# Kernel tuning notes

Measured on AMD Instinct MI355X. Metric: run time of the kernel, lower is better.

The kernel has to match this reference:

```python
import jax, jax.numpy as jnp
import numpy as np
import math

VOCAB = 32000
HIDDEN = 256
N_HEADS = 8
HEAD_DIM = 32
MAX_LEN = 2048


def _pos_encoding(max_len, d_model, dtype=jnp.float32):
    # Matches PositionalEncoding buffer (even d_model).
    pos = jnp.arange(max_len, dtype=dtype)[:, None]                       # [L,1]
    div = jnp.exp(jnp.arange(0, d_model, 2, dtype=dtype) * (-(math.log(10000.0) / d_model)))
    ang = pos * div                                                        # [L, d/2]
    pe = jnp.zeros((max_len, d_model), dtype=dtype)
    pe = pe.at[:, 0::2].set(jnp.sin(ang))
    pe = pe.at[:, 1::2].set(jnp.cos(ang))
    return pe


def setup_inputs() -> dict:
    key = jax.random.key(0)
    ks = jax.random.split(key, 7)
    B, S = 8, 2047
    s = 0.02
    x = jax.random.randint(ks[0], (B, S), 0, VOCAB + 1, dtype=jnp.int64)
    emb_w = jax.random.normal(ks[1], (VOCAB + 1, HIDDEN), jnp.float32) * s
    wq = jax.random.normal(ks[2], (N_HEADS, HEAD_DIM, HIDDEN), jnp.float32) * s
    wk = jax.random.normal(ks[3], (N_HEADS, HEAD_DIM, HIDDEN), jnp.float32) * s
    wv = jax.random.normal(ks[4], (N_HEADS, HEAD_DIM, HIDDEN), jnp.float32) * s
    wo = jax.random.normal(ks[5], (HIDDEN, N_HEADS * HEAD_DIM), jnp.float32) * s
    wu = jax.random.normal(ks[6], (VOCAB + 1, HIDDEN), jnp.float32) * s
    return {"x": x, "emb_w": emb_w, "wq": wq, "wk": wk, "wv": wv, "wo": wo, "wu": wu}


def reference(x, emb_w, wq, wk, wv, wo, wu):
    B, S = x.shape
    # prepend CLS token (id=2)
    tok = jnp.concatenate([jnp.full((B, 1), 2, dtype=x.dtype), x], axis=1)  # [B, S+1]
    y = emb_w[tok]                                                          # [B, S+1, H]
    y = y + _pos_encoding(S + 1, HIDDEN, y.dtype)
    # batched per-head QKV (nn.Linear: out = in @ W.T)
    q = jnp.einsum('bsh,nkh->bnsk', y, wq)
    k = jnp.einsum('bsh,nkh->bnsk', y, wk)
    v = jnp.einsum('bsh,nkh->bnsk', y, wv)
    scores = jnp.einsum('bnsk,bntk->bnst', q, k) / (HEAD_DIM ** 0.5)        # [B,N,S+1,S+1]
    A = jax.nn.softmax(scores, axis=-1)
    o = jnp.einsum('bnst,bntk->bnsk', A, v)                                 # [B,N,S+1,K]
    o = jnp.transpose(o, (0, 2, 1, 3)).reshape(B, S + 1, N_HEADS * HEAD_DIM)
    att = o @ wo.T + y     # residual inside MultiHeadAttention
    y = att + y            # second residual in MultiHeadTransformerPosEmb.forward
    out = y[:, 0, :] @ wu.T                                                 # [B, VOCAB+1]
    return out
```

## Files before the change

kernel.cpp:

```cpp
#include <hip/hip_runtime.h>
#include <stdint.h>

#define B_   8
#define S_   2047
#define L_   2048
#define H_   256
#define NH_  8
#define HD_  32
#define V_   32001
#define NCH_ 128
#define TCH_ 16
#define GRID_ 1024
#define BAR_STRIDE_ 2048

__device__ __forceinline__ void ast(float* p, float v) {
    __hip_atomic_store((unsigned int*)p, __float_as_uint(v),
                       __ATOMIC_RELAXED, __HIP_MEMORY_SCOPE_AGENT);
}
__device__ __forceinline__ float ald(const float* p) {
    return __uint_as_float(__hip_atomic_load((const unsigned int*)p,
                           __ATOMIC_RELAXED, __HIP_MEMORY_SCOPE_AGENT));
}
__device__ __forceinline__ float foldx(float a, int off) {
    return a + __shfl_xor(a, off, 64);
}
__device__ __forceinline__ float sel8(const float a[8], int j) {
    float v = a[0];
    v = (j == 1) ? a[1] : v;
    v = (j == 2) ? a[2] : v;
    v = (j == 3) ? a[3] : v;
    v = (j == 4) ? a[4] : v;
    v = (j == 5) ? a[5] : v;
    v = (j == 6) ? a[6] : v;
    v = (j == 7) ? a[7] : v;
    return v;
}

__device__ __forceinline__ void gsync(unsigned int* bp, int bid) {
    __syncthreads();
    if (threadIdx.x == 0) {
        int sg = bid & 31;
        unsigned int* sub = bp + 16 + sg * 16;
        unsigned int* rel = bp + 528 + sg * 16;
        unsigned int prev = __hip_atomic_fetch_add(sub, 1u, __ATOMIC_RELAXED,
                                                   __HIP_MEMORY_SCOPE_AGENT);
        if (prev == 31u) {
            unsigned int m = __hip_atomic_fetch_add(bp, 1u, __ATOMIC_RELAXED,
                                                    __HIP_MEMORY_SCOPE_AGENT);
            if (m == 31u) {
                for (int i = 0; i < 32; ++i)
                    __hip_atomic_store(bp + 528 + i * 16, 1u, __ATOMIC_RELAXED,
                                       __HIP_MEMORY_SCOPE_AGENT);
            }
        }
        while (__hip_atomic_load(rel, __ATOMIC_RELAXED,
                                 __HIP_MEMORY_SCOPE_AGENT) == 0u)
            __builtin_amdgcn_s_sleep(2);
    }
    __syncthreads();
}

__global__ __launch_bounds__(256, 4) void mega(const int* __restrict__ x,
                                               const float* __restrict__ emb,
                                               const float* __restrict__ wq,
                                               const float* __restrict__ wk,
                                               const float* __restrict__ wv,
                                               const float* __restrict__ wo,
                                               const float* __restrict__ wu,
                                               float* __restrict__ out,
                                               float* __restrict__ qk,
                                               float* __restrict__ z,
                                               float* __restrict__ o_g,
                                               float* __restrict__ esum_blk,
                                               float* __restrict__ psum,
                                               unsigned int* __restrict__ bars) {
    int bid = blockIdx.x, tid = threadIdx.x;

    __shared__ float smem[4][2056];
    float* smf = &smem[0][0];

    if (bid < NH_) {
        int n = bid;
        float* y0l = smem[0];
        float* q0p = smem[1];
        float* q0l = smem[2];
        float v = emb[2 * H_ + tid] + ((tid & 1) ? 1.0f : 0.0f);
        y0l[tid] = v;
        __syncthreads();
        {
            int k = tid >> 3, part = tid & 7;
            const float* w = wq + (n * HD_ + k) * H_ + part * 32;
            const float* yy = y0l + part * 32;
            float acc = 0.f;
#pragma unroll
            for (int j = 0; j < 32; ++j) acc += w[j] * yy[j];
            q0p[k * 8 + part] = acc;
        }
        __syncthreads();
        if (tid < HD_) {
            float s = 0.f;
#pragma unroll
            for (int j = 0; j < 8; ++j) s += q0p[tid * 8 + j];
            q0l[tid] = s;
        }
        __syncthreads();
        float acc = 0.f;
        for (int k = 0; k < HD_; ++k)
            acc += q0l[k] * wk[(n * HD_ + k) * H_ + tid];
        ast(qk + n * H_ + tid, acc * 0.17677669529663687f);
    }
    gsync(bars + 0 * BAR_STRIDE_, bid);

    {
        int b = bid >> 7, c = bid & 127;
        int lane = tid & 63, w = tid >> 6;
        int h0 = lane * 4;

        for (int i = tid; i < NH_ * H_; i += 256)
            smem[3][i] = ald(qk + i);
        __syncthreads();

        float4 qr[NH_];
#pragma unroll
        for (int n = 0; n < NH_; ++n)
            qr[n] = *(const float4*)&smem[3][n * H_ + h0];
        __syncthreads();

        const float cdiv = 0.07195578414202881f;
        float div0 = __expf(-(float)(lane * 2) * cdiv);
        float div1 = __expf(-(float)(lane * 2 + 1) * cdiv);

        float4 acc[NH_];
        float es[NH_];
#pragma unroll
        for (int n = 0; n < NH_; ++n) {
            acc[n] = make_float4(0.f, 0.f, 0.f, 0.f);
            es[n] = 0.f;
        }

        int t0 = c * TCH_ + w * 4;
        int toks[4];
#pragma unroll
        for (int i = 0; i < 4; ++i) {
            int t = t0 + i;
            toks[i] = (t == 0) ? 2 : x[b * S_ + t - 1];
        }

#pragma unroll
        for (int i = 0; i < 4; ++i) {
            int t = t0 + i;
            float4 ev = *(const float4*)(emb + (size_t)toks[i] * H_ + h0);
            float a0 = (float)t * div0, a1 = (float)t * div1;
            float4 y4;
            y4.x = ev.x + __sinf(a0); y4.y = ev.y + __cosf(a0);
            y4.z = ev.z + __sinf(a1); y4.w = ev.w + __cosf(a1);

            float a[NH_];
#pragma unroll
            for (int n = 0; n < NH_; ++n)
                a[n] = qr[n].x * y4.x + qr[n].y * y4.y + qr[n].z * y4.z + qr[n].w * y4.w;

            float m4[4];
#pragma unroll
            for (int k = 0; k < 4; ++k) {
                float lo = foldx(a[k], 32), hi = foldx(a[k + 4], 32);
                m4[k] = (lane & 32) ? hi : lo;
            }
            float m2[2];
#pragma unroll
            for (int k = 0; k < 2; ++k) {
                float lo = foldx(m4[k], 16), hi = foldx(m4[k + 2], 16);
                m2[k] = (lane & 16) ? hi : lo;
            }
            float lo = foldx(m2[0], 8), hi = foldx(m2[1], 8);
            float m1 = (lane & 8) ? hi : lo;
            m1 = foldx(m1, 4); m1 = foldx(m1, 2); m1 = foldx(m1, 1);
            float e = __expf(m1);

#pragma unroll
            for (int n = 0; n < NH_; ++n) {
                float en = __shfl(e, n * 8, 64);
                acc[n].x += en * y4.x; acc[n].y += en * y4.y;
                acc[n].z += en * y4.z; acc[n].w += en * y4.w;
                es[n] += en;
            }
        }

#pragma unroll
        for (int n = 0; n < NH_; ++n)
            *(float4*)&smem[w][n * H_ + h0] = acc[n];
        if (lane < NH_) smem[w][2048 + lane] = sel8(es, lane);
        __syncthreads();

#pragma unroll
        for (int jj = 0; jj < (NH_ * H_) / 256; ++jj) {
            int j = jj * 256 + tid;
            ast(psum + (size_t)bid * (NH_ * H_) + j,
                smem[0][j] + smem[1][j] + smem[2][j] + smem[3][j]);
        }
        if (tid < NH_)
            ast(esum_blk + bid * NH_ + tid,
                smem[0][2048 + tid] + smem[1][2048 + tid]
              + smem[2][2048 + tid] + smem[3][2048 + tid]);
    }
    gsync(bars + 1 * BAR_STRIDE_, bid);

    if (bid < 64) {
        int b = bid >> 3, n = bid & 7;
        float* ybar  = smem[0];
        float* opb   = smem[1];
        float* es128 = smem[2];
        if (tid < 128)
            es128[tid] = ald(esum_blk + (size_t)(b * NCH_ + tid) * NH_ + n);
        __syncthreads();
        if (tid < 64) {
            float v = es128[tid] + es128[tid + 64];
#pragma unroll
            for (int off = 32; off > 0; off >>= 1) v += __shfl_xor(v, off, 64);
            if (tid == 0) es128[192] = 1.0f / v;
        }
        __syncthreads();
        {
            const float* pp = psum + (size_t)(b * NCH_) * (NH_ * H_) + n * H_ + tid;
            float s = 0.f;
#pragma unroll 16
            for (int cc = 0; cc < NCH_; ++cc) s += ald(pp + (size_t)cc * NH_ * H_);
            ybar[tid] = s * es128[192];
        }
        __syncthreads();
        {
            int k = tid >> 3, p = tid & 7;
            const float* wrow = wv + (size_t)(n * HD_ + k) * H_ + p * 32;
            const float* yy = ybar + p * 32;
            float s = 0.f;
#pragma unroll
            for (int j = 0; j < 32; ++j) s += wrow[j] * yy[j];
            opb[k * 8 + p] = s;
        }
        __syncthreads();
        if (tid < HD_) {
            float s = 0.f;
#pragma unroll
            for (int p = 0; p < 8; ++p) s += opb[tid * 8 + p];
            ast(o_g + b * (NH_ * HD_) + n * HD_ + tid, s);
        }
    }
    gsync(bars + 2 * BAR_STRIDE_, bid);

    if (bid < B_) {
        int b = bid;
        float* o_l = smem[0];
        o_l[tid] = ald(o_g + b * (NH_ * HD_) + tid);
        float y0v = emb[2 * H_ + tid] + ((tid & 1) ? 1.0f : 0.0f);
        __syncthreads();
        const float* wrow = wo + (size_t)tid * (NH_ * HD_);
        float s = 0.f;
#pragma unroll 16
        for (int j4 = 0; j4 < (NH_ * HD_) / 4; ++j4) {
            float4 w4 = *(const float4*)(wrow + j4 * 4);
            s += w4.x * o_l[j4 * 4] + w4.y * o_l[j4 * 4 + 1]
               + w4.z * o_l[j4 * 4 + 2] + w4.w * o_l[j4 * 4 + 3];
        }
        ast(z + b * H_ + tid, s + 2.0f * y0v);
    }
    gsync(bars + 3 * BAR_STRIDE_, bid);

    if (bid < (V_ + 63) / 64) {
        int lane = tid & 63, w = tid >> 6;
        int m = lane & 15;
        int g = lane >> 4;
        float* zs = smf;
        float* sm_out = smf + 2560;
        for (int i = tid; i < B_ * H_; i += 256) {
            int b = i >> 8, h = i & 255;
            zs[b * 320 + (h >> 4) * 20 + (h & 15)] = ald(z + i);
        }
        __syncthreads();

        int base = bid * 64;
#pragma unroll
        for (int pass = 0; pass < 4; ++pass) {
            int rl = w * 16 + pass * 4 + g;
            int v = base + rl;
            int vc = (v < V_) ? v : (V_ - 1);
            const float* wr = wu + (size_t)vc * H_ + m * 16;
            float4 w0 = *(const float4*)(wr);
            float4 w1 = *(const float4*)(wr + 4);
            float4 w2 = *(const float4*)(wr + 8);
            float4 w3 = *(const float4*)(wr + 12);
            float acc[B_];
#pragma unroll
            for (int b = 0; b < B_; ++b) {
                const float* zb = zs + b * 320 + m * 20;
                float4 z0 = *(const float4*)(zb);
                float4 z1 = *(const float4*)(zb + 4);
                float4 z2 = *(const float4*)(zb + 8);
                float4 z3 = *(const float4*)(zb + 12);
                acc[b] = z0.x * w0.x + z0.y * w0.y + z0.z * w0.z + z0.w * w0.w
                       + z1.x * w1.x + z1.y * w1.y + z1.z * w1.z + z1.w * w1.w
                       + z2.x * w2.x + z2.y * w2.y + z2.z * w2.z + z2.w * w2.w
                       + z3.x * w3.x + z3.y * w3.y + z3.z * w3.z + z3.w * w3.w;
            }
#pragma unroll
            for (int off = 1; off <= 8; off <<= 1) {
#pragma unroll
                for (int b = 0; b < B_; ++b) acc[b] += __shfl_xor(acc[b], off, 64);
            }
            if (m < B_) sm_out[m * 65 + rl] = sel8(acc, m);
        }
        __syncthreads();
        for (int i = tid; i < B_ * 64; i += 256) {
            int b = i >> 6, vl = i & 63, v = base + vl;
            if (v < V_) out[b * V_ + v] = sm_out[b * 65 + vl];
        }
    }
}

extern "C" void kernel_launch(void* const* d_in, const int* in_sizes, int n_in,
                              void* d_out, int out_size, void* d_ws, size_t ws_size,
                              hipStream_t stream) {
    const int*   x   = (const int*)d_in[0];
    const float* emb = (const float*)d_in[1];
    const float* wq  = (const float*)d_in[2];
    const float* wk  = (const float*)d_in[3];
    const float* wv  = (const float*)d_in[4];
    const float* wo  = (const float*)d_in[5];
    const float* wu  = (const float*)d_in[6];
    float*       out = (float*)d_out;

    float* qk       = (float*)d_ws;
    float* z        = qk + NH_ * H_;
    float* o_g      = z + B_ * H_;
    float* esum_blk = o_g + B_ * NH_ * HD_;
    float* psum     = esum_blk + GRID_ * NH_;
    unsigned int* bars = (unsigned int*)(psum + (size_t)GRID_ * NH_ * H_);

    hipMemsetAsync(bars, 0, 4 * BAR_STRIDE_ * sizeof(unsigned int), stream);

    mega<<<GRID_, 256, 0, stream>>>(x, emb, wq, wk, wv, wo, wu, out,
                                    qk, z, o_g, esum_blk, psum, bars);
}
```

Measured before the change: 146.9 us.

## Replace grid-wide barriers with targeted flag waits and double grid size

Removes the four full-grid barriers. Each stage now signals its consumers through counters or release flags, so blocks wait only on the data they need, and the unembedding weight rows are prefetched before the wait. The grid doubles to 2048 blocks with 8 tokens each and occupancy 8, and per-wave accumulators are replaced by LDS atomics. This raises occupancy and overlap, but spin-waiting depends on every block being co-resident, and the LDS atomics plus twice as many partial sums add contention and reduction work.

```diff
diff --git a/kernel.cpp b/kernel.cpp
--- a/kernel.cpp
+++ b/kernel.cpp
@@ -8,9 +8,9 @@
 #define NH_  8
 #define HD_  32
 #define V_   32001
-#define NCH_ 128
-#define TCH_ 16
-#define GRID_ 1024
+#define NCH_ 256
+#define TCH_ 8
+#define GRID_ 2048
 #define BAR_STRIDE_ 2048
 
 __device__ __forceinline__ void ast(float* p, float v) {
@@ -20,6 +20,12 @@
 __device__ __forceinline__ float ald(const float* p) {
     return __uint_as_float(__hip_atomic_load((const unsigned int*)p,
                            __ATOMIC_RELAXED, __HIP_MEMORY_SCOPE_AGENT));
+}
+__device__ __forceinline__ unsigned aadd(unsigned* p) {
+    return __hip_atomic_fetch_add(p, 1u, __ATOMIC_RELAXED, __HIP_MEMORY_SCOPE_AGENT);
+}
+__device__ __forceinline__ unsigned aldu(const unsigned* p) {
+    return __hip_atomic_load(p, __ATOMIC_RELAXED, __HIP_MEMORY_SCOPE_AGENT);
 }
 __device__ __forceinline__ float foldx(float a, int off) {
     return a + __shfl_xor(a, off, 64);
@@ -36,31 +42,7 @@
     return v;
 }
 
-__device__ __forceinline__ void gsync(unsigned int* bp, int bid) {
-    __syncthreads();
-    if (threadIdx.x == 0) {
-        int sg = bid & 31;
-        unsigned int* sub = bp + 16 + sg * 16;
-        unsigned int* rel = bp + 528 + sg * 16;
-        unsigned int prev = __hip_atomic_fetch_add(sub, 1u, __ATOMIC_RELAXED,
-                                                   __HIP_MEMORY_SCOPE_AGENT);
-        if (prev == 31u) {
-            unsigned int m = __hip_atomic_fetch_add(bp, 1u, __ATOMIC_RELAXED,
-                                                    __HIP_MEMORY_SCOPE_AGENT);
-            if (m == 31u) {
-                for (int i = 0; i < 32; ++i)
-                    __hip_atomic_store(bp + 528 + i * 16, 1u, __ATOMIC_RELAXED,
-                                       __HIP_MEMORY_SCOPE_AGENT);
-            }
-        }
-        while (__hip_atomic_load(rel, __ATOMIC_RELAXED,
-                                 __HIP_MEMORY_SCOPE_AGENT) == 0u)
-            __builtin_amdgcn_s_sleep(2);
-    }
-    __syncthreads();
-}
-
-__global__ __launch_bounds__(256, 4) void mega(const int* __restrict__ x,
+__global__ __launch_bounds__(256, 8) void mega(const int* __restrict__ x,
                                                const float* __restrict__ emb,
                                                const float* __restrict__ wq,
                                                const float* __restrict__ wk,
@@ -76,14 +58,19 @@
                                                unsigned int* __restrict__ bars) {
     int bid = blockIdx.x, tid = threadIdx.x;
 
-    __shared__ float smem[4][2056];
-    float* smf = &smem[0][0];
+    __shared__ float smBig[4096];
+    __shared__ float esA[NH_];
+
+    unsigned* qbar  = bars;
+    unsigned* acnt  = bars + BAR_STRIDE_;
+    unsigned* b1cnt = bars + 2 * BAR_STRIDE_;
+    unsigned* zbar  = bars + 3 * BAR_STRIDE_;
 
     if (bid < NH_) {
         int n = bid;
-        float* y0l = smem[0];
-        float* q0p = smem[1];
-        float* q0l = smem[2];
+        float* y0l = smBig;
+        float* q0p = smBig + 256;
+        float* q0l = smBig + 512;
         float v = emb[2 * H_ + tid] + ((tid & 1) ? 1.0f : 0.0f);
         y0l[tid] = v;
         __syncthreads();
@@ -108,48 +95,48 @@
         for (int k = 0; k < HD_; ++k)
             acc += q0l[k] * wk[(n * HD_ + k) * H_ + tid];
         ast(qk + n * H_ + tid, acc * 0.17677669529663687f);
-    }
-    gsync(bars + 0 * BAR_STRIDE_, bid);
+        __syncthreads();
+        if (tid == 0) {
+            if (aadd(qbar) == NH_ - 1) {
+                for (int i = 0; i < 32; ++i)
+                    __hip_atomic_store(qbar + 528 + i * 16, 1u,
+                                       __ATOMIC_RELAXED, __HIP_MEMORY_SCOPE_AGENT);
+            }
+        }
+    }
 
     {
-        int b = bid >> 7, c = bid & 127;
+        int b = bid >> 8, c = bid & 255;
         int lane = tid & 63, w = tid >> 6;
         int h0 = lane * 4;
-
-        for (int i = tid; i < NH_ * H_; i += 256)
-            smem[3][i] = ald(qk + i);
-        __syncthreads();
-
-        float4 qr[NH_];
-#pragma unroll
-        for (int n = 0; n < NH_; ++n)
-            qr[n] = *(const float4*)&smem[3][n * H_ + h0];
-        __syncthreads();
-
+        int t0 = c * TCH_ + w * 2;
+
+        int tok0 = (t0 == 0) ? 2 : x[b * S_ + t0 - 1];
+        int tok1 = x[b * S_ + t0];
+        float4 ev0 = *(const float4*)(emb + (size_t)tok0 * H_ + h0);
+        float4 ev1 = *(const float4*)(emb + (size_t)tok1 * H_ + h0);
         const float cdiv = 0.07195578414202881f;
         float div0 = __expf(-(float)(lane * 2) * cdiv);
         float div1 = __expf(-(float)(lane * 2 + 1) * cdiv);
 
-        float4 acc[NH_];
-        float es[NH_];
-#pragma unroll
-        for (int n = 0; n < NH_; ++n) {
-            acc[n] = make_float4(0.f, 0.f, 0.f, 0.f);
-            es[n] = 0.f;
-        }
-
-        int t0 = c * TCH_ + w * 4;
-        int toks[4];
-#pragma unroll
-        for (int i = 0; i < 4; ++i) {
-            int t = t0 + i;
-            toks[i] = (t == 0) ? 2 : x[b * S_ + t - 1];
-        }
-
-#pragma unroll
-        for (int i = 0; i < 4; ++i) {
-            int t = t0 + i;
-            float4 ev = *(const float4*)(emb + (size_t)toks[i] * H_ + h0);
+        for (int i = tid; i < NH_ * H_; i += 256) smBig[i] = 0.f;
+        if (tid < NH_) esA[tid] = 0.f;
+        __builtin_amdgcn_sched_barrier(0);
+
+        if (tid == 0) {
+            while (aldu(qbar + 528 + (bid & 31) * 16) == 0u)
+                __builtin_amdgcn_s_sleep(2);
+        }
+        __syncthreads();
+
+        float* qk_l = smBig + 2048;
+        for (int i = tid; i < NH_ * H_; i += 256) qk_l[i] = ald(qk + i);
+        __syncthreads();
+
+#pragma unroll
+        for (int it = 0; it < 2; ++it) {
+            int t = t0 + it;
+            float4 ev = it ? ev1 : ev0;
             float a0 = (float)t * div0, a1 = (float)t * div1;
             float4 y4;
             y4.x = ev.x + __sinf(a0); y4.y = ev.y + __cosf(a0);
@@ -157,9 +144,10 @@
 
             float a[NH_];
 #pragma unroll
-            for (int n = 0; n < NH_; ++n)
-                a[n] = qr[n].x * y4.x + qr[n].y * y4.y + qr[n].z * y4.z + qr[n].w * y4.w;
-
+            for (int n = 0; n < NH_; ++n) {
+                float4 q4 = *(const float4*)&qk_l[n * H_ + h0];
+                a[n] = q4.x * y4.x + q4.y * y4.y + q4.z * y4.z + q4.w * y4.w;
+            }
             float m4[4];
 #pragma unroll
             for (int k = 0; k < 4; ++k) {
@@ -180,52 +168,50 @@
 #pragma unroll
             for (int n = 0; n < NH_; ++n) {
                 float en = __shfl(e, n * 8, 64);
-                acc[n].x += en * y4.x; acc[n].y += en * y4.y;
-                acc[n].z += en * y4.z; acc[n].w += en * y4.w;
-                es[n] += en;
-            }
-        }
-
-#pragma unroll
-        for (int n = 0; n < NH_; ++n)
-            *(float4*)&smem[w][n * H_ + h0] = acc[n];
-        if (lane < NH_) smem[w][2048 + lane] = sel8(es, lane);
+                atomicAdd(&smBig[n * H_ + h0 + 0], en * y4.x);
+                atomicAdd(&smBig[n * H_ + h0 + 1], en * y4.y);
+                atomicAdd(&smBig[n * H_ + h0 + 2], en * y4.z);
+                atomicAdd(&smBig[n * H_ + h0 + 3], en * y4.w);
+            }
+            if ((lane & 7) == 0) atomicAdd(&esA[lane >> 3], e);
+        }
         __syncthreads();
 
 #pragma unroll
         for (int jj = 0; jj < (NH_ * H_) / 256; ++jj) {
             int j = jj * 256 + tid;
-            ast(psum + (size_t)bid * (NH_ * H_) + j,
-                smem[0][j] + smem[1][j] + smem[2][j] + smem[3][j]);
-        }
-        if (tid < NH_)
-            ast(esum_blk + bid * NH_ + tid,
-                smem[0][2048 + tid] + smem[1][2048 + tid]
-              + smem[2][2048 + tid] + smem[3][2048 + tid]);
-    }
-    gsync(bars + 1 * BAR_STRIDE_, bid);
-
-    if (bid < 64) {
-        int b = bid >> 3, n = bid & 7;
-        float* ybar  = smem[0];
-        float* opb   = smem[1];
-        float* es128 = smem[2];
-        if (tid < 128)
-            es128[tid] = ald(esum_blk + (size_t)(b * NCH_ + tid) * NH_ + n);
+            ast(psum + (size_t)bid * (NH_ * H_) + j, smBig[j]);
+        }
+        if (tid < NH_) ast(esum_blk + bid * NH_ + tid, esA[tid]);
+        __syncthreads();
+        if (tid == 0) aadd(acnt);
+    }
+
+    if (bid >= GRID_ - 64) {
+        int id = bid - (GRID_ - 64);
+        int b = id >> 3, n = id & 7;
+        if (tid == 0) {
+            while (aldu(acnt) < (unsigned)GRID_) __builtin_amdgcn_s_sleep(2);
+        }
+        __syncthreads();
+        float* es_l = smBig;
+        float* ybar = smBig + 256;
+        float* opb  = smBig + 512;
+        es_l[tid] = ald(esum_blk + (size_t)(b * NCH_ + tid) * NH_ + n);
         __syncthreads();
         if (tid < 64) {
-            float v = es128[tid] + es128[tid + 64];
+            float v = es_l[tid] + es_l[tid + 64] + es_l[tid + 128] + es_l[tid + 192];
 #pragma unroll
             for (int off = 32; off > 0; off >>= 1) v += __shfl_xor(v, off, 64);
-            if (tid == 0) es128[192] = 1.0f / v;
+            if (tid == 0) smBig[768] = 1.0f / v;
         }
         __syncthreads();
         {
             const float* pp = psum + (size_t)(b * NCH_) * (NH_ * H_) + n * H_ + tid;
             float s = 0.f;
 #pragma unroll 16
-            for (int cc = 0; cc < NCH_; ++cc) s += ald(pp + (size_t)cc * NH_ * H_);
-            ybar[tid] = s * es128[192];
+            for (int cc = 0; cc < NCH_; ++cc) s += ald(pp + (size_t)cc * (NH_ * H_));
+            ybar[tid] = s * smBig[768];
         }
         __syncthreads();
         {
@@ -244,12 +230,17 @@
             for (int p = 0; p < 8; ++p) s += opb[tid * 8 + p];
             ast(o_g + b * (NH_ * HD_) + n * HD_ + tid, s);
         }
-    }
-    gsync(bars + 2 * BAR_STRIDE_, bid);
-
-    if (bid < B_) {
-        int b = bid;
-        float* o_l = smem[0];
+        __syncthreads();
+        if (tid == 0) aadd(b1cnt);
+    }
+
+    if (bid >= GRID_ - 8) {
+        int b = bid - (GRID_ - 8);
+        if (tid == 0) {
+            while (aldu(b1cnt) < 64u) __builtin_amdgcn_s_sleep(2);
+        }
+        __syncthreads();
+        float* o_l = smBig;
         o_l[tid] = ald(o_g + b * (NH_ * HD_) + tid);
         float y0v = emb[2 * H_ + tid] + ((tid & 1) ? 1.0f : 0.0f);
         __syncthreads();
@@ -262,56 +253,67 @@
                + w4.z * o_l[j4 * 4 + 2] + w4.w * o_l[j4 * 4 + 3];
         }
         ast(z + b * H_ + tid, s + 2.0f * y0v);
-    }
-    gsync(bars + 3 * BAR_STRIDE_, bid);
-
-    if (bid < (V_ + 63) / 64) {
+        __syncthreads();
+        if (tid == 0) {
+            if (aadd(zbar) == 7u) {
+                for (int i = 0; i < 32; ++i)
+                    __hip_atomic_store(zbar + 528 + i * 16, 1u,
+                                       __ATOMIC_RELAXED, __HIP_MEMORY_SCOPE_AGENT);
+            }
+        }
+    }
+
+    {
         int lane = tid & 63, w = tid >> 6;
-        int m = lane & 15;
-        int g = lane >> 4;
-        float* zs = smf;
-        float* sm_out = smf + 2560;
+        int m = lane & 15, g = lane >> 4;
+        int base = bid * 16;
+        int rl = w * 4 + g;
+        int v = base + rl;
+        int vc = (v < V_) ? v : (V_ - 1);
+        const float* wr = wu + (size_t)vc * H_ + m * 16;
+        float4 w0 = *(const float4*)(wr);
+        float4 w1 = *(const float4*)(wr + 4);
+        float4 w2 = *(const float4*)(wr + 8);
+        float4 w3 = *(const float4*)(wr + 12);
+        __builtin_amdgcn_sched_barrier(0);
+
+        if (tid == 0) {
+            while (aldu(zbar + 528 + (bid & 31) * 16) == 0u)
+                __builtin_amdgcn_s_sleep(4);
+        }
+        __syncthreads();
+
+        float* zs = smBig;
+        float* sm_out = smBig + 2560;
         for (int i = tid; i < B_ * H_; i += 256) {
-            int b = i >> 8, h = i & 255;
-            zs[b * 320 + (h >> 4) * 20 + (h & 15)] = ald(z + i);
-        }
-        __syncthreads();
-
-        int base = bid * 64;
-#pragma unroll
-        for (int pass = 0; pass < 4; ++pass) {
-            int rl = w * 16 + pass * 4 + g;
-            int v = base + rl;
-            int vc = (v < V_) ? v : (V_ - 1);
-            const float* wr = wu + (size_t)vc * H_ + m * 16;
-            float4 w0 = *(const float4*)(wr);
-            float4 w1 = *(const float4*)(wr + 4);
-            float4 w2 = *(const float4*)(wr + 8);
-            float4 w3 = *(const float4*)(wr + 12);
-            float acc[B_];
-#pragma unroll
-            for (int b = 0; b < B_; ++b) {
-                const float* zb = zs + b * 320 + m * 20;
-                float4 z0 = *(const float4*)(zb);
-                float4 z1 = *(const float4*)(zb + 4);
-                float4 z2 = *(const float4*)(zb + 8);
-                float4 z3 = *(const float4*)(zb + 12);
-                acc[b] = z0.x * w0.x + z0.y * w0.y + z0.z * w0.z + z0.w * w0.w
-                       + z1.x * w1.x + z1.y * w1.y + z1.z * w1.z + z1.w * w1.w
-                       + z2.x * w2.x + z2.y * w2.y + z2.z * w2.z + z2.w * w2.w
-                       + z3.x * w3.x + z3.y * w3.y + z3.z * w3.z + z3.w * w3.w;
-            }
-#pragma unroll
-            for (int off = 1; off <= 8; off <<= 1) {
-#pragma unroll
-                for (int b = 0; b < B_; ++b) acc[b] += __shfl_xor(acc[b], off, 64);
-            }
-            if (m < B_) sm_out[m * 65 + rl] = sel8(acc, m);
-        }
-        __syncthreads();
-        for (int i = tid; i < B_ * 64; i += 256) {
-            int b = i >> 6, vl = i & 63, v = base + vl;
-            if (v < V_) out[b * V_ + v] = sm_out[b * 65 + vl];
+            int bb = i >> 8, h = i & 255;
+            zs[bb * 320 + (h >> 4) * 20 + (h & 15)] = ald(z + i);
+        }
+        __syncthreads();
+
+        float acc[B_];
+#pragma unroll
+        for (int bb = 0; bb < B_; ++bb) {
+            const float* zb = zs + bb * 320 + m * 20;
+            float4 z0 = *(const float4*)(zb);
+            float4 z1 = *(const float4*)(zb + 4);
+            float4 z2 = *(const float4*)(zb + 8);
+            float4 z3 = *(const float4*)(zb + 12);
+            acc[bb] = z0.x * w0.x + z0.y * w0.y + z0.z * w0.z + z0.w * w0.w
+                    + z1.x * w1.x + z1.y * w1.y + z1.z * w1.z + z1.w * w1.w
+                    + z2.x * w2.x + z2.y * w2.y + z2.z * w2.z + z2.w * w2.w
+                    + z3.x * w3.x + z3.y * w3.y + z3.z * w3.z + z3.w * w3.w;
+        }
+#pragma unroll
+        for (int off = 1; off <= 8; off <<= 1) {
+#pragma unroll
+            for (int bb = 0; bb < B_; ++bb) acc[bb] += __shfl_xor(acc[bb], off, 64);
+        }
+        if (m < B_) sm_out[m * 17 + rl] = sel8(acc, m);
+        __syncthreads();
+        if (tid < B_ * 16) {
+            int bb = tid >> 4, vl = tid & 15, vv = base + vl;
+            if (vv < V_) out[bb * V_ + vv] = sm_out[bb * 17 + vl];
         }
     }
 }
@@ -332,7 +334,7 @@
     float* z        = qk + NH_ * H_;
     float* o_g      = z + B_ * H_;
     float* esum_blk = o_g + B_ * NH_ * HD_;
-    float* psum     = esum_blk + GRID_ * NH_;
+    float* psum     = esum_blk + (size_t)GRID_ * NH_;
     unsigned int* bars = (unsigned int*)(psum + (size_t)GRID_ * NH_ * H_);
 
     hipMemsetAsync(bars, 0, 4 * BAR_STRIDE_ * sizeof(unsigned int), stream);
```

After: 314.2 us. +113.8%, slower.

## Replace grid barriers with targeted flags, atomic partial sums, and prefetch before waits

Applied to the files above, without the earlier changes.

Swaps the four full-grid barriers for point-to-point flags. Only the 8 q-producer blocks signal the attention stage, a counter gates the 8 reduction blocks, and the 8 z-producer blocks release the vocab stage. Per-chunk partial sums are now accumulated with float atomicAdd into per-batch buffers instead of being written per block and summed later, and the V and O projections are fused into one stage. Embedding rows and the first unembedding weights are loaded before each wait so their latency overlaps synchronization, and the vocab projection is spread over all 1024 blocks at 32 rows each. In exchange, atomic contention on the shared sums rises and floating-point summation order becomes nondeterministic.

```diff
diff --git a/kernel.cpp b/kernel.cpp
--- a/kernel.cpp
+++ b/kernel.cpp
@@ -21,6 +21,15 @@
     return __uint_as_float(__hip_atomic_load((const unsigned int*)p,
                            __ATOMIC_RELAXED, __HIP_MEMORY_SCOPE_AGENT));
 }
+__device__ __forceinline__ unsigned aadd(unsigned* p) {
+    return __hip_atomic_fetch_add(p, 1u, __ATOMIC_RELAXED, __HIP_MEMORY_SCOPE_AGENT);
+}
+__device__ __forceinline__ unsigned aldu(const unsigned* p) {
+    return __hip_atomic_load(p, __ATOMIC_RELAXED, __HIP_MEMORY_SCOPE_AGENT);
+}
+__device__ __forceinline__ void vdrain() {
+    asm volatile("s_waitcnt vmcnt(0)" ::: "memory");
+}
 __device__ __forceinline__ float foldx(float a, int off) {
     return a + __shfl_xor(a, off, 64);
 }
@@ -36,30 +45,6 @@
     return v;
 }
 
-__device__ __forceinline__ void gsync(unsigned int* bp, int bid) {
-    __syncthreads();
-    if (threadIdx.x == 0) {
-        int sg = bid & 31;
-        unsigned int* sub = bp + 16 + sg * 16;
-        unsigned int* rel = bp + 528 + sg * 16;
-        unsigned int prev = __hip_atomic_fetch_add(sub, 1u, __ATOMIC_RELAXED,
-                                                   __HIP_MEMORY_SCOPE_AGENT);
-        if (prev == 31u) {
-            unsigned int m = __hip_atomic_fetch_add(bp, 1u, __ATOMIC_RELAXED,
-                                                    __HIP_MEMORY_SCOPE_AGENT);
-            if (m == 31u) {
-                for (int i = 0; i < 32; ++i)
-                    __hip_atomic_store(bp + 528 + i * 16, 1u, __ATOMIC_RELAXED,
-                                       __HIP_MEMORY_SCOPE_AGENT);
-            }
-        }
-        while (__hip_atomic_load(rel, __ATOMIC_RELAXED,
-                                 __HIP_MEMORY_SCOPE_AGENT) == 0u)
-            __builtin_amdgcn_s_sleep(2);
-    }
-    __syncthreads();
-}
-
 __global__ __launch_bounds__(256, 4) void mega(const int* __restrict__ x,
                                                const float* __restrict__ emb,
                                                const float* __restrict__ wq,
@@ -70,14 +55,17 @@
                                                float* __restrict__ out,
                                                float* __restrict__ qk,
                                                float* __restrict__ z,
-                                               float* __restrict__ o_g,
-                                               float* __restrict__ esum_blk,
-                                               float* __restrict__ psum,
+                                               float* __restrict__ obar,
+                                               float* __restrict__ ebar,
                                                unsigned int* __restrict__ bars) {
     int bid = blockIdx.x, tid = threadIdx.x;
 
     __shared__ float smem[4][2056];
     float* smf = &smem[0][0];
+
+    unsigned* qbar = bars;
+    unsigned* acnt = bars + BAR_STRIDE_;
+    unsigned* zbar = bars + 2 * BAR_STRIDE_;
 
     if (bid < NH_) {
         int n = bid;
@@ -108,27 +96,53 @@
         for (int k = 0; k < HD_; ++k)
             acc += q0l[k] * wk[(n * HD_ + k) * H_ + tid];
         ast(qk + n * H_ + tid, acc * 0.17677669529663687f);
+        vdrain();
+        __syncthreads();
+        if (tid == 0) {
+            if (aadd(qbar) == NH_ - 1) {
+                for (int i = 0; i < 32; ++i)
+                    __hip_atomic_store(qbar + 528 + i * 16, 1u,
+                                       __ATOMIC_RELAXED, __HIP_MEMORY_SCOPE_AGENT);
+            }
+        }
+        __syncthreads();
     }
-    gsync(bars + 0 * BAR_STRIDE_, bid);
 
     {
         int b = bid >> 7, c = bid & 127;
         int lane = tid & 63, w = tid >> 6;
         int h0 = lane * 4;
-
-        for (int i = tid; i < NH_ * H_; i += 256)
-            smem[3][i] = ald(qk + i);
-        __syncthreads();
-
-        float4 qr[NH_];
-#pragma unroll
-        for (int n = 0; n < NH_; ++n)
-            qr[n] = *(const float4*)&smem[3][n * H_ + h0];
-        __syncthreads();
-
+        int t0 = c * TCH_ + w * 4;
+
+        int toks[4];
+#pragma unroll
+        for (int i = 0; i < 4; ++i) {
+            int t = t0 + i;
+            toks[i] = (t == 0) ? 2 : x[b * S_ + t - 1];
+        }
+        float4 evr[4];
+#pragma unroll
+        for (int i = 0; i < 4; ++i)
+            evr[i] = *(const float4*)(emb + (size_t)toks[i] * H_ + h0);
         const float cdiv = 0.07195578414202881f;
         float div0 = __expf(-(float)(lane * 2) * cdiv);
         float div1 = __expf(-(float)(lane * 2 + 1) * cdiv);
+        __builtin_amdgcn_sched_barrier(0);
+
+        if (tid == 0) {
+            while (aldu(qbar + 528 + (bid & 31) * 16) == 0u)
+                __builtin_amdgcn_s_sleep(2);
+        }
+        __syncthreads();
+
+        for (int i = tid; i < NH_ * H_; i += 256)
+            smem[3][i] = ald(qk + i);
+        __syncthreads();
+        float4 qr[NH_];
+#pragma unroll
+        for (int n = 0; n < NH_; ++n)
+            qr[n] = *(const float4*)&smem[3][n * H_ + h0];
+        __syncthreads();
 
         float4 acc[NH_];
         float es[NH_];
@@ -138,18 +152,10 @@
             es[n] = 0.f;
         }
 
-        int t0 = c * TCH_ + w * 4;
-        int toks[4];
 #pragma unroll
         for (int i = 0; i < 4; ++i) {
             int t = t0 + i;
-            toks[i] = (t == 0) ? 2 : x[b * S_ + t - 1];
-        }
-
-#pragma unroll
-        for (int i = 0; i < 4; ++i) {
-            int t = t0 + i;
-            float4 ev = *(const float4*)(emb + (size_t)toks[i] * H_ + h0);
+            float4 ev = evr[i];
             float a0 = (float)t * div0, a1 = (float)t * div1;
             float4 y4;
             y4.x = ev.x + __sinf(a0); y4.y = ev.y + __cosf(a0);
@@ -195,123 +201,137 @@
 #pragma unroll
         for (int jj = 0; jj < (NH_ * H_) / 256; ++jj) {
             int j = jj * 256 + tid;
-            ast(psum + (size_t)bid * (NH_ * H_) + j,
-                smem[0][j] + smem[1][j] + smem[2][j] + smem[3][j]);
+            atomicAdd(obar + b * (NH_ * H_) + j,
+                      smem[0][j] + smem[1][j] + smem[2][j] + smem[3][j]);
         }
         if (tid < NH_)
-            ast(esum_blk + bid * NH_ + tid,
-                smem[0][2048 + tid] + smem[1][2048 + tid]
-              + smem[2][2048 + tid] + smem[3][2048 + tid]);
+            atomicAdd(ebar + b * NH_ + tid,
+                      smem[0][2048 + tid] + smem[1][2048 + tid]
+                    + smem[2][2048 + tid] + smem[3][2048 + tid]);
+        vdrain();
+        __syncthreads();
+        if (tid == 0) aadd(acnt);
     }
-    gsync(bars + 1 * BAR_STRIDE_, bid);
-
-    if (bid < 64) {
-        int b = bid >> 3, n = bid & 7;
-        float* ybar  = smem[0];
-        float* opb   = smem[1];
-        float* es128 = smem[2];
-        if (tid < 128)
-            es128[tid] = ald(esum_blk + (size_t)(b * NCH_ + tid) * NH_ + n);
-        __syncthreads();
-        if (tid < 64) {
-            float v = es128[tid] + es128[tid + 64];
-#pragma unroll
-            for (int off = 32; off > 0; off >>= 1) v += __shfl_xor(v, off, 64);
-            if (tid == 0) es128[192] = 1.0f / v;
-        }
+
+    if (bid >= 8 && bid < 16) {
+        int b = bid - 8;
+        if (tid == 0) {
+            while (aldu(acnt) < (unsigned)GRID_) __builtin_amdgcn_s_sleep(2);
+        }
+        __syncthreads();
+        float* ybar_l = smf;
+        float* o_l    = smf + 2048;
+        float* sB     = smf + 2304;
+        if (tid < NH_) sB[tid] = 1.0f / ald(ebar + b * NH_ + tid);
+        __syncthreads();
+        for (int i = tid; i < NH_ * H_; i += 256)
+            ybar_l[i] = ald(obar + b * (NH_ * H_) + i) * sB[i >> 8];
         __syncthreads();
         {
-            const float* pp = psum + (size_t)(b * NCH_) * (NH_ * H_) + n * H_ + tid;
+            int n = tid >> 5;
+            const float* wrow = wv + (size_t)tid * H_;
+            const float* yy = ybar_l + n * H_;
             float s = 0.f;
 #pragma unroll 16
-            for (int cc = 0; cc < NCH_; ++cc) s += ald(pp + (size_t)cc * NH_ * H_);
-            ybar[tid] = s * es128[192];
+            for (int j4 = 0; j4 < H_ / 4; ++j4) {
+                float4 w4 = *(const float4*)(wrow + j4 * 4);
+                s += w4.x * yy[j4 * 4] + w4.y * yy[j4 * 4 + 1]
+                   + w4.z * yy[j4 * 4 + 2] + w4.w * yy[j4 * 4 + 3];
+            }
+            o_l[tid] = s;
         }
         __syncthreads();
         {
-            int k = tid >> 3, p = tid & 7;
-            const float* wrow = wv + (size_t)(n * HD_ + k) * H_ + p * 32;
-            const float* yy = ybar + p * 32;
+            float y0v = emb[2 * H_ + tid] + ((tid & 1) ? 1.0f : 0.0f);
+            const float* wrow = wo + (size_t)tid * (NH_ * HD_);
             float s = 0.f;
-#pragma unroll
-            for (int j = 0; j < 32; ++j) s += wrow[j] * yy[j];
-            opb[k * 8 + p] = s;
-        }
-        __syncthreads();
-        if (tid < HD_) {
-            float s = 0.f;
-#pragma unroll
-            for (int p = 0; p < 8; ++p) s += opb[tid * 8 + p];
-            ast(o_g + b * (NH_ * HD_) + n * HD_ + tid, s);
-        }
+#pragma unroll 16
+            for (int j4 = 0; j4 < (NH_ * HD_) / 4; ++j4) {
+                float4 w4 = *(const float4*)(wrow + j4 * 4);
+                s += w4.x * o_l[j4 * 4] + w4.y * o_l[j4 * 4 + 1]
+                   + w4.z * o_l[j4 * 4 + 2] + w4.w * o_l[j4 * 4 + 3];
+            }
+            ast(z + b * H_ + tid, s + 2.0f * y0v);
+        }
+        vdrain();
+        __syncthreads();
+        if (tid == 0) {
+            if (aadd(zbar) == B_ - 1) {
+                for (int i = 0; i < 32; ++i)
+                    __hip_atomic_store(zbar + 528 + i * 16, 1u,
+                                       __ATOMIC_RELAXED, __HIP_MEMORY_SCOPE_AGENT);
+            }
+        }
+        __syncthreads();
     }
-    gsync(bars + 2 * BAR_STRIDE_, bid);
-
-    if (bid < B_) {
-        int b = bid;
-        float* o_l = smem[0];
-        o_l[tid] = ald(o_g + b * (NH_ * HD_) + tid);
-        float y0v = emb[2 * H_ + tid] + ((tid & 1) ? 1.0f : 0.0f);
-        __syncthreads();
-        const float* wrow = wo + (size_t)tid * (NH_ * HD_);
-        float s = 0.f;
-#pragma unroll 16
-        for (int j4 = 0; j4 < (NH_ * HD_) / 4; ++j4) {
-            float4 w4 = *(const float4*)(wrow + j4 * 4);
-            s += w4.x * o_l[j4 * 4] + w4.y * o_l[j4 * 4 + 1]
-               + w4.z * o_l[j4 * 4 + 2] + w4.w * o_l[j4 * 4 + 3];
-        }
-        ast(z + b * H_ + tid, s + 2.0f * y0v);
-    }
-    gsync(bars + 3 * BAR_STRIDE_, bid);
-
-    if (bid < (V_ + 63) / 64) {
+
+    {
         int lane = tid & 63, w = tid >> 6;
-        int m = lane & 15;
-        int g = lane >> 4;
+        int m = lane & 15, g = lane >> 4;
+        int base = bid * 32;
+
+        int rl0 = w * 4 + g;
+        int v0 = base + rl0;
+        int vc0 = (v0 < V_) ? v0 : (V_ - 1);
+        const float* wr0 = wu + (size_t)vc0 * H_ + m * 16;
+        float4 p00 = *(const float4*)(wr0);
+        float4 p01 = *(const float4*)(wr0 + 4);
+        float4 p02 = *(const float4*)(wr0 + 8);
+        float4 p03 = *(const float4*)(wr0 + 12);
+        __builtin_amdgcn_sched_barrier(0);
+
+        if (tid == 0) {
+            while (aldu(zbar + 528 + (bid & 31) * 16) == 0u)
+                __builtin_amdgcn_s_sleep(2);
+        }
+        __syncthreads();
+
         float* zs = smf;
         float* sm_out = smf + 2560;
         for (int i = tid; i < B_ * H_; i += 256) {
-            int b = i >> 8, h = i & 255;
-            zs[b * 320 + (h >> 4) * 20 + (h & 15)] = ald(z + i);
-        }
-        __syncthreads();
-
-        int base = bid * 64;
-#pragma unroll
-        for (int pass = 0; pass < 4; ++pass) {
-            int rl = w * 16 + pass * 4 + g;
-            int v = base + rl;
-            int vc = (v < V_) ? v : (V_ - 1);
-            const float* wr = wu + (size_t)vc * H_ + m * 16;
-            float4 w0 = *(const float4*)(wr);
-            float4 w1 = *(const float4*)(wr + 4);
-            float4 w2 = *(const float4*)(wr + 8);
-            float4 w3 = *(const float4*)(wr + 12);
+            int bb = i >> 8, h = i & 255;
+            zs[bb * 320 + (h >> 4) * 20 + (h & 15)] = ald(z + i);
+        }
+        __syncthreads();
+
+#pragma unroll
+        for (int pass = 0; pass < 2; ++pass) {
+            int rl = pass * 16 + w * 4 + g;
+            float4 w0, w1, w2, w3;
+            if (pass == 0) { w0 = p00; w1 = p01; w2 = p02; w3 = p03; }
+            else {
+                int v = base + rl;
+                int vc = (v < V_) ? v : (V_ - 1);
+                const float* wr = wu + (size_t)vc * H_ + m * 16;
+                w0 = *(const float4*)(wr);
+                w1 = *(const float4*)(wr + 4);
+                w2 = *(const float4*)(wr + 8);
+                w3 = *(const float4*)(wr + 12);
+            }
             float acc[B_];
 #pragma unroll
-            for (int b = 0; b < B_; ++b) {
-                const float* zb = zs + b * 320 + m * 20;
+            for (int bb = 0; bb < B_; ++bb) {
+                const float* zb = zs + bb * 320 + m * 20;
                 float4 z0 = *(const float4*)(zb);
                 float4 z1 = *(const float4*)(zb + 4);
                 float4 z2 = *(const float4*)(zb + 8);
                 float4 z3 = *(const float4*)(zb + 12);
-                acc[b] = z0.x * w0.x + z0.y * w0.y + z0.z * w0.z + z0.w * w0.w
-                       + z1.x * w1.x + z1.y * w1.y + z1.z * w1.z + z1.w * w1.w
-                       + z2.x * w2.x + z2.y * w2.y + z2.z * w2.z + z2.w * w2.w
-                       + z3.x * w3.x + z3.y * w3.y + z3.z * w3.z + z3.w * w3.w;
+                acc[bb] = z0.x * w0.x + z0.y * w0.y + z0.z * w0.z + z0.w * w0.w
+                        + z1.x * w1.x + z1.y * w1.y + z1.z * w1.z + z1.w * w1.w
+                        + z2.x * w2.x + z2.y * w2.y + z2.z * w2.z + z2.w * w2.w
+                        + z3.x * w3.x + z3.y * w3.y + z3.z * w3.z + z3.w * w3.w;
             }
 #pragma unroll
             for (int off = 1; off <= 8; off <<= 1) {
 #pragma unroll
-                for (int b = 0; b < B_; ++b) acc[b] += __shfl_xor(acc[b], off, 64);
-            }
-            if (m < B_) sm_out[m * 65 + rl] = sel8(acc, m);
-        }
-        __syncthreads();
-        for (int i = tid; i < B_ * 64; i += 256) {
-            int b = i >> 6, vl = i & 63, v = base + vl;
-            if (v < V_) out[b * V_ + v] = sm_out[b * 65 + vl];
+                for (int bb = 0; bb < B_; ++bb) acc[bb] += __shfl_xor(acc[bb], off, 64);
+            }
+            if (m < B_) sm_out[m * 33 + rl] = sel8(acc, m);
+        }
+        __syncthreads();
+        {
+            int bb = tid >> 5, vl = tid & 31, vv = base + vl;
+            if (vv < V_) out[bb * V_ + vv] = sm_out[bb * 33 + vl];
         }
     }
 }
@@ -328,15 +348,16 @@
     const float* wu  = (const float*)d_in[6];
     float*       out = (float*)d_out;
 
-    float* qk       = (float*)d_ws;
-    float* z        = qk + NH_ * H_;
-    float* o_g      = z + B_ * H_;
-    float* esum_blk = o_g + B_ * NH_ * HD_;
-    float* psum     = esum_blk + GRID_ * NH_;
-    unsigned int* bars = (unsigned int*)(psum + (size_t)GRID_ * NH_ * H_);
-
-    hipMemsetAsync(bars, 0, 4 * BAR_STRIDE_ * sizeof(unsigned int), stream);
+    float* qk   = (float*)d_ws;
+    float* z    = qk + NH_ * H_;
+    float* obar = z + B_ * H_;
+    float* ebar = obar + B_ * NH_ * H_;
+    unsigned int* bars = (unsigned int*)(ebar + B_ * NH_);
+
+    hipMemsetAsync(obar, 0,
+                   (B_ * NH_ * H_ + B_ * NH_) * sizeof(float)
+                 + 3 * BAR_STRIDE_ * sizeof(unsigned int), stream);
 
     mega<<<GRID_, 256, 0, stream>>>(x, emb, wq, wk, wv, wo, wu, out,
-                                    qk, z, o_g, esum_blk, psum, bars);
-}
+                                    qk, z, obar, ebar, bars);
+}
```

Result: slower. 160.7 us (+9.4%).
